# Kernel tuning notes

Hardware: AMD Instinct MI355X
Metric: run time of the kernel (lower is better)

## Reference

```python
import jax, jax.numpy as jnp
import numpy as np

B, G, D, H, L, FFN = 4, 2048, 256, 8, 4, 1024
HD = D // H
BASE = 100.0
MASK_ID = -10.0
LN_EPS = 1e-5


def setup_inputs() -> dict:
    key = jax.random.key(0)
    ks = jax.random.split(key, 18)
    s = 0.02
    f32 = jnp.float32
    return {
        "x": jax.random.uniform(ks[0], (B, G), f32, 0.0, 8.0),
        "gene_emb": jax.random.normal(ks[1], (G, D), f32) * s,
        "Wq": jax.random.normal(ks[2], (L, D, D), f32) * s,
        "bq": jnp.zeros((L, D), f32),
        "Wk": jax.random.normal(ks[3], (L, D, D), f32) * s,
        "bk": jnp.zeros((L, D), f32),
        "Wv": jax.random.normal(ks[4], (L, D, D), f32) * s,
        "bv": jnp.zeros((L, D), f32),
        "ln1_g": jnp.ones((L, D), f32),
        "ln1_b": jnp.zeros((L, D), f32),
        "ln2_g": jnp.ones((L, D), f32),
        "ln2_b": jnp.zeros((L, D), f32),
        "WU": jax.random.normal(ks[5], (L, D, FFN), f32) * s,
        "bU": jnp.zeros((L, FFN), f32),
        "WV": jax.random.normal(ks[6], (L, FFN, D), f32) * s,
        "bV": jnp.zeros((L, D), f32),
        "Wo": jax.random.normal(ks[7], (D, 1), f32) * s,
        "bo": jnp.zeros((1,), f32),
    }


def _ln(x, g, b):
    mu = jnp.mean(x, axis=-1, keepdims=True)
    var = jnp.mean(jnp.square(x - mu), axis=-1, keepdims=True)
    return (x - mu) * jax.lax.rsqrt(var + LN_EPS) * g + b


def _linear_attn(z, Wq, bq, Wk, bk, Wv, bv):
    # feature_type='sqr': phi(u) = u**2; causal (compute_type='iter') linear attention
    q = jnp.square(z @ Wq + bq).reshape(B, G, H, HD)
    k = jnp.square(z @ Wk + bk).reshape(B, G, H, HD)
    v = (z @ Wv + bv).reshape(B, G, H, HD)
    kv = jnp.cumsum(jnp.einsum('bshm,bshd->bshmd', k, v), axis=1)  # prefix sums of k (x) v
    ksum = jnp.cumsum(k, axis=1)
    num = jnp.einsum('bshm,bshmd->bshd', q, kv)
    den = jnp.einsum('bshm,bshm->bsh', q, ksum)
    return (num / (den[..., None] + 1e-16)).reshape(B, G, D)


def reference(x, gene_emb, Wq, bq, Wk, bk, Wv, bv, ln1_g, ln1_b, ln2_g, ln2_b,
              WU, bU, WV, bV, Wo, bo):
    # rotary expression embedding
    inv_freq = 1.0 / BASE ** (jnp.arange(0, D, 2, dtype=jnp.float32) / D)  # [D/2]
    freqs = x[:, :, None] * inv_freq                                       # [B,G,D/2]
    ree = jnp.concatenate([jnp.sin(freqs), jnp.cos(freqs)], axis=-1)       # [B,G,D]
    ree = jnp.where((x == MASK_ID)[..., None], 0.0, ree)
    h = gene_emb[None] + ree
    for l in range(L):
        # pre-LN attention block
        h = h + _linear_attn(_ln(h, ln1_g[l], ln1_b[l]), Wq[l], bq[l], Wk[l], bk[l], Wv[l], bv[l])
        # pre-LN FFN block (exact erf gelu, as torch F.gelu default)
        z = _ln(h, ln2_g[l], ln2_b[l])
        h = h + jax.nn.gelu(z @ WU[l] + bU[l], approximate=False) @ WV[l] + bV[l]
    return (h @ Wo + bo)[..., 0]  # [B,G]
```

## Files before the change

### kernel.cpp

```cpp
#include <hip/hip_runtime.h>
#include <math.h>

constexpr int kB = 4, kG = 2048, kD = 256, kH = 8, kHD = 32, kL = 4, kFFN = 1024;
constexpr int kBG = kB * kG;
constexpr int kCHUNK = 64;
constexpr int kNC = kG / kCHUNK;
constexpr int kSUMSZ = kHD * kHD + kHD;
constexpr int kQKVN = 3 * kD;

typedef __bf16 bf16x8 __attribute__((ext_vector_type(8)));
typedef unsigned short ushort8 __attribute__((ext_vector_type(8)));
typedef float floatx4 __attribute__((ext_vector_type(4)));

__device__ __forceinline__ unsigned short f2bf(float f) {
  unsigned int u = __float_as_uint(f);
  u += 0x7fff + ((u >> 16) & 1);
  return (unsigned short)(u >> 16);
}

__device__ __forceinline__ void load_lds_16(const void* g, void* l) {
  __builtin_amdgcn_global_load_lds((const __attribute__((address_space(1))) void*)g,
                                   (__attribute__((address_space(3))) void*)l,
                                   16, 0, 0);
}

__global__ void embed_kernel(const float* __restrict__ x,
                             const float* __restrict__ ge,
                             float* __restrict__ h) {
  int idx = blockIdx.x * 256 + threadIdx.x;
  int d = idx & (kD - 1);
  int g = (idx >> 8) & (kG - 1);
  int b = idx >> 19;
  float xv = x[b * kG + g];
  int i = d & 127;
  float inv = expf(-(float)i * (4.6051701859880914f / 128.0f));
  float f = xv * inv;
  float r = (d < 128) ? sinf(f) : cosf(f);
  if (xv == -10.0f) r = 0.0f;
  h[idx] = ge[g * kD + d] + r;
}

__global__ void convert_weights_kernel(
    const float* __restrict__ Wq, const float* __restrict__ Wk,
    const float* __restrict__ Wv, const float* __restrict__ WU,
    const float* __restrict__ WV, const float* __restrict__ bq,
    const float* __restrict__ bk, const float* __restrict__ bv,
    unsigned short* __restrict__ Wqkv_t, unsigned short* __restrict__ WU_t,
    unsigned short* __restrict__ WV_t, float* __restrict__ bias_qkv) {
  int blk = blockIdx.x;
  if (blk >= kL * 704) {
    int idx = (blk - kL * 704) * 256 + threadIdx.x;
    if (idx < kL * kQKVN) {
      int l = idx / kQKVN, n = idx % kQKVN;
      float v = (n < 256) ? bq[l * 256 + n]
              : (n < 512) ? bk[l * 256 + n - 256]
                          : bv[l * 256 + n - 512];
      bias_qkv[idx] = v;
    }
    return;
  }
  int l = blk / 704, id = blk % 704;
  const float* src;
  unsigned short* dst;
  int Ksrc, Nsrc, kt, nt;
  if (id < 192) {
    int m = id >> 6, tid = id & 63;
    src = (m == 0 ? Wq : m == 1 ? Wk : Wv) + (size_t)l * 256 * 256;
    dst = Wqkv_t + (size_t)l * kQKVN * 256 + (size_t)m * 256 * 256;
    Ksrc = 256; Nsrc = 256; kt = tid >> 3; nt = tid & 7;
  } else if (id < 448) {
    int tid = id - 192;
    src = WU + (size_t)l * 256 * 1024;
    dst = WU_t + (size_t)l * 1024 * 256;
    Ksrc = 256; Nsrc = 1024; kt = tid >> 5; nt = tid & 31;
  } else {
    int tid = id - 448;
    src = WV + (size_t)l * 1024 * 256;
    dst = WV_t + (size_t)l * 256 * 1024;
    Ksrc = 1024; Nsrc = 256; kt = tid >> 3; nt = tid & 7;
  }
  __shared__ float s[32][33];
  int tx = threadIdx.x & 31, ty = threadIdx.x >> 5;
#pragma unroll
  for (int r = 0; r < 4; r++)
    s[ty + r * 8][tx] = src[(size_t)(kt * 32 + ty + r * 8) * Nsrc + nt * 32 + tx];
  __syncthreads();
#pragma unroll
  for (int r = 0; r < 4; r++)
    dst[(size_t)(nt * 32 + ty + r * 8) * Ksrc + kt * 32 + tx] =
        f2bf(s[tx][ty + r * 8]);
}

__global__ __launch_bounds__(256) void ln_kernel(
    const float* __restrict__ h, const float* __restrict__ gamma,
    const float* __restrict__ beta, unsigned short* __restrict__ z) {
  int w = threadIdx.x >> 6, lane = threadIdx.x & 63;
  size_t row = (size_t)blockIdx.x * 4 + w;
  float4 v = *(const float4*)&h[row * kD + lane * 4];
  float s = v.x + v.y + v.z + v.w;
  float sq = v.x * v.x + v.y * v.y + v.z * v.z + v.w * v.w;
#pragma unroll
  for (int o = 32; o > 0; o >>= 1) {
    s += __shfl_xor(s, o);
    sq += __shfl_xor(sq, o);
  }
  float mu = s * (1.0f / kD);
  float var = sq * (1.0f / kD) - mu * mu;
  float r = rsqrtf(var + 1e-5f);
  float4 g4 = *(const float4*)&gamma[lane * 4];
  float4 b4 = *(const float4*)&beta[lane * 4];
  float y0 = (v.x - mu) * r * g4.x + b4.x;
  float y1 = (v.y - mu) * r * g4.y + b4.y;
  float y2 = (v.z - mu) * r * g4.z + b4.z;
  float y3 = (v.w - mu) * r * g4.w + b4.w;
  unsigned int u0 = (unsigned int)f2bf(y0) | ((unsigned int)f2bf(y1) << 16);
  unsigned int u1 = (unsigned int)f2bf(y2) | ((unsigned int)f2bf(y3) << 16);
  uint2 uu; uu.x = u0; uu.y = u1;
  *(uint2*)&z[row * kD + lane * 4] = uu;
}

template <int EPI>
__global__ __launch_bounds__(256) void mfma_gemm(
    const unsigned short* __restrict__ A, const unsigned short* __restrict__ Bt,
    const float* __restrict__ bias, void* __restrict__ Cout,
    const float* __restrict__ Cres, int M, int N, int K) {
  __shared__ unsigned short As[2][64 * 32];
  __shared__ unsigned short Bs[2][64 * 32];
  const int t = threadIdx.x;
  const int w = t >> 6, lane = t & 63;
  const int bm = blockIdx.y * 64, bn = blockIdx.x * 64;
  const int wm = (w >> 1) * 32, wn = (w & 1) * 32;

  const int srow = lane >> 2;
  const int skof = (lane & 3) * 8;
  const unsigned short* ap = A + (size_t)(bm + w * 16 + srow) * K + skof;
  const unsigned short* bp = Bt + (size_t)(bn + w * 16 + srow) * K + skof;

  floatx4 acc[2][2];
#pragma unroll
  for (int i = 0; i < 2; i++)
#pragma unroll
    for (int j = 0; j < 2; j++) acc[i][j] = (floatx4){0.f, 0.f, 0.f, 0.f};

  const int lm = lane & 15, lq = lane >> 4;
  const int nsteps = K >> 5;

  load_lds_16(ap, &As[0][w * 512]);
  load_lds_16(bp, &Bs[0][w * 512]);
  __syncthreads();

  for (int s = 0; s < nsteps; s++) {
    const int cur = s & 1, nxt = cur ^ 1;
    if (s + 1 < nsteps) {
      load_lds_16(ap + (s + 1) * 32, &As[nxt][w * 512]);
      load_lds_16(bp + (s + 1) * 32, &Bs[nxt][w * 512]);
    }
    const unsigned short* afp = &As[cur][(wm + lm) * 32 + lq * 8];
    const unsigned short* bfp = &Bs[cur][(wn + lm) * 32 + lq * 8];
    bf16x8 af[2], bfr[2];
#pragma unroll
    for (int i = 0; i < 2; i++)
      af[i] = __builtin_bit_cast(bf16x8,
          *reinterpret_cast<const ushort8*>(afp + i * 16 * 32));
#pragma unroll
    for (int j = 0; j < 2; j++)
      bfr[j] = __builtin_bit_cast(bf16x8,
          *reinterpret_cast<const ushort8*>(bfp + j * 16 * 32));
#pragma unroll
    for (int i = 0; i < 2; i++)
#pragma unroll
      for (int j = 0; j < 2; j++)
        acc[i][j] = __builtin_amdgcn_mfma_f32_16x16x32_bf16(af[i], bfr[j],
                                                            acc[i][j], 0, 0, 0);
    __syncthreads();
  }

  const int r0 = bm + wm + lq * 4;
  const int c0 = bn + wn + lm;
#pragma unroll
  for (int j = 0; j < 2; j++) {
    int col = c0 + j * 16;
    float bv = bias[col];
#pragma unroll
    for (int i = 0; i < 2; i++) {
      int rowb = r0 + i * 16;
#pragma unroll
      for (int r = 0; r < 4; r++) {
        int row = rowb + r;
        float v = acc[i][j][r] + bv;
        size_t idx = (size_t)row * N + col;
        if (EPI == 1) {
          ((float*)Cout)[idx] = (col < 512) ? v * v : v;
        } else if (EPI == 2) {
          float g = 0.5f * v * (1.0f + erff(v * 0.70710678118654752f));
          ((unsigned short*)Cout)[idx] = f2bf(g);
        } else {
          ((float*)Cout)[idx] = Cres[idx] + v;
        }
      }
    }
  }
}

__global__ __launch_bounds__(256) void attn_sums_kernel(
    const float* __restrict__ qkv, float* __restrict__ sums) {
  int blk = blockIdx.x;
  int c = blk & (kNC - 1);
  int hh = (blk >> 5) & (kH - 1);
  int b = blk >> 8;
  int g0 = c * kCHUNK;
  __shared__ float ks[kCHUNK][kHD];
  __shared__ float vs[kCHUNK][kHD];
  const float* kbase = qkv + (size_t)(b * kG + g0) * kQKVN + 256 + hh * kHD;
  const float* vbase = qkv + (size_t)(b * kG + g0) * kQKVN + 512 + hh * kHD;
#pragma unroll
  for (int r = 0; r < 2; r++) {
    int e = threadIdx.x + r * 256;
    int i = e >> 3, j = (e & 7) * 4;
    *(float4*)&ks[i][j] = *(const float4*)&kbase[(size_t)i * kQKVN + j];
    *(float4*)&vs[i][j] = *(const float4*)&vbase[(size_t)i * kQKVN + j];
  }
  __syncthreads();
  int m = threadIdx.x >> 3, n0 = (threadIdx.x & 7) * 4;
  float a0 = 0, a1 = 0, a2 = 0, a3 = 0;
  for (int i = 0; i < kCHUNK; i++) {
    float km = ks[i][m];
    float4 v4 = *(const float4*)&vs[i][n0];
    a0 = fmaf(km, v4.x, a0); a1 = fmaf(km, v4.y, a1);
    a2 = fmaf(km, v4.z, a2); a3 = fmaf(km, v4.w, a3);
  }
  float* outp = sums + (size_t)blk * kSUMSZ;
  *(float4*)&outp[m * kHD + n0] = make_float4(a0, a1, a2, a3);
  if (threadIdx.x < kHD) {
    float s = 0;
    for (int i = 0; i < kCHUNK; i++) s += ks[i][threadIdx.x];
    outp[kHD * kHD + threadIdx.x] = s;
  }
}

__global__ void attn_scan_kernel(float* __restrict__ sums) {
  int bh = blockIdx.x / 5, part = blockIdx.x % 5;
  int e = part * 256 + threadIdx.x;
  if (e >= kSUMSZ) return;
  float* base = sums + (size_t)bh * kNC * kSUMSZ + e;
  float v[kNC];
#pragma unroll
  for (int c = 0; c < kNC; c++) v[c] = base[(size_t)c * kSUMSZ];
  float run = 0;
#pragma unroll
  for (int c = 0; c < kNC; c++) {
    float tv = v[c];
    base[(size_t)c * kSUMSZ] = run;
    run += tv;
  }
}

__global__ __launch_bounds__(256) void attn_out_kernel(
    const float* __restrict__ qkv, const float* __restrict__ sums,
    float* __restrict__ h) {
  int blk = blockIdx.x;
  int c = blk & (kNC - 1);
  int hh = (blk >> 5) & (kH - 1);
  int b = blk >> 8;
  int g0 = c * kCHUNK;
  __shared__ float qs[kCHUNK][36];
  __shared__ float ks[kCHUNK][36];
  __shared__ float vs[kCHUNK][36];
  __shared__ float Sf[kHD][kHD];
  __shared__ float ksum[kHD];
  __shared__ float dinv_s[kCHUNK];
  __shared__ float Amat[kCHUNK][68];
  int t = threadIdx.x;
  const float* base = qkv + (size_t)(b * kG + g0) * kQKVN + hh * kHD;
#pragma unroll
  for (int r = 0; r < 2; r++) {
    int e = t + r * 256;
    int i = e >> 3, j = (e & 7) * 4;
    *(float4*)&qs[i][j] = *(const float4*)&base[(size_t)i * kQKVN + j];
    *(float4*)&ks[i][j] = *(const float4*)&base[(size_t)i * kQKVN + 256 + j];
    *(float4*)&vs[i][j] = *(const float4*)&base[(size_t)i * kQKVN + 512 + j];
  }
  const float* sp = sums + (size_t)blk * kSUMSZ;
  *(float4*)&((float*)Sf)[t * 4] = *(const float4*)&sp[t * 4];
  if (t < 8) *(float4*)&ksum[t * 4] = *(const float4*)&sp[kHD * kHD + t * 4];
  __syncthreads();

  {
    int i = t >> 2, jb = t & 3;
    float qr[kHD];
#pragma unroll
    for (int m4 = 0; m4 < kHD / 4; m4++) {
      float4 qv = *(const float4*)&qs[i][m4 * 4];
      qr[m4 * 4 + 0] = qv.x; qr[m4 * 4 + 1] = qv.y;
      qr[m4 * 4 + 2] = qv.z; qr[m4 * 4 + 3] = qv.w;
    }
    float psum = 0.0f;
#pragma unroll
    for (int jj = 0; jj < 16; jj++) {
      int j = jb + jj * 4;
      float s = 0;
#pragma unroll
      for (int m4 = 0; m4 < kHD / 4; m4++) {
        float4 kv = *(const float4*)&ks[j][m4 * 4];
        s = fmaf(qr[m4 * 4 + 0], kv.x, s);
        s = fmaf(qr[m4 * 4 + 1], kv.y, s);
        s = fmaf(qr[m4 * 4 + 2], kv.z, s);
        s = fmaf(qr[m4 * 4 + 3], kv.w, s);
      }
      Amat[i][j] = s;
      if (j <= i) psum += s;
    }
    psum += __shfl_xor(psum, 1);
    psum += __shfl_xor(psum, 2);
    if (jb == 0) {
      float dk = 0;
#pragma unroll
      for (int m = 0; m < kHD; m++) dk = fmaf(qr[m], ksum[m], dk);
      dinv_s[i] = 1.0f / (psum + dk + 1e-16f);
    }
  }
  __syncthreads();

  float* hbase = h + (size_t)(b * kG + g0) * kD + hh * kHD;
#pragma unroll
  for (int uu = 0; uu < 2; uu++) {
    int u = t + uu * 256;
    int i = u >> 3, n0 = (u & 7) * 4;
    float ax = 0, ay = 0, az = 0, aw = 0;
#pragma unroll
    for (int m = 0; m < kHD; m++) {
      float qm = qs[i][m];
      float4 s4 = *(const float4*)&Sf[m][n0];
      ax = fmaf(qm, s4.x, ax); ay = fmaf(qm, s4.y, ay);
      az = fmaf(qm, s4.z, az); aw = fmaf(qm, s4.w, aw);
    }
    for (int j = 0; j <= i; j++) {
      float w = Amat[i][j];
      float4 vv = *(const float4*)&vs[j][n0];
      ax = fmaf(w, vv.x, ax); ay = fmaf(w, vv.y, ay);
      az = fmaf(w, vv.z, az); aw = fmaf(w, vv.w, aw);
    }
    float dinv = dinv_s[i];
    float* hp = hbase + (size_t)i * kD + n0;
    float4 old = *(const float4*)hp;
    *(float4*)hp = make_float4(old.x + ax * dinv, old.y + ay * dinv,
                               old.z + az * dinv, old.w + aw * dinv);
  }
}

__global__ __launch_bounds__(256) void final_kernel(
    const float* __restrict__ h, const float* __restrict__ Wo,
    const float* __restrict__ bo, float* __restrict__ out) {
  int w = threadIdx.x >> 6, lane = threadIdx.x & 63;
  size_t row = (size_t)blockIdx.x * 4 + w;
  float4 hv = *(const float4*)&h[row * kD + lane * 4];
  float4 wv = *(const float4*)&Wo[lane * 4];
  float s = hv.x * wv.x + hv.y * wv.y + hv.z * wv.z + hv.w * wv.w;
#pragma unroll
  for (int o = 32; o > 0; o >>= 1) s += __shfl_xor(s, o);
  if (lane == 0) out[row] = s + bo[0];
}

extern "C" void kernel_launch(void* const* d_in, const int* in_sizes, int n_in,
                              void* d_out, int out_size, void* d_ws, size_t ws_size,
                              hipStream_t stream) {
  const float* x    = (const float*)d_in[0];
  const float* ge   = (const float*)d_in[1];
  const float* Wq   = (const float*)d_in[2];
  const float* bq   = (const float*)d_in[3];
  const float* Wk   = (const float*)d_in[4];
  const float* bk   = (const float*)d_in[5];
  const float* Wv   = (const float*)d_in[6];
  const float* bv   = (const float*)d_in[7];
  const float* ln1g = (const float*)d_in[8];
  const float* ln1b = (const float*)d_in[9];
  const float* ln2g = (const float*)d_in[10];
  const float* ln2b = (const float*)d_in[11];
  const float* WU   = (const float*)d_in[12];
  const float* bU   = (const float*)d_in[13];
  const float* WV   = (const float*)d_in[14];
  const float* bV   = (const float*)d_in[15];
  const float* Wo   = (const float*)d_in[16];
  const float* bo   = (const float*)d_in[17];
  float* out = (float*)d_out;

  float* ws = (float*)d_ws;
  float*          h       = ws;
  unsigned short* zb      = (unsigned short*)(ws + 2097152);
  float*          qkv     = ws + 3145728;
  unsigned short* u       = (unsigned short*)qkv;
  float*          sums    = ws + 9437184;
  unsigned short* Wqkv_t  = (unsigned short*)(ws + 10518528);
  unsigned short* WU_t    = (unsigned short*)(ws + 10911744);
  unsigned short* WV_t    = (unsigned short*)(ws + 11436032);
  float*          bias_qkv= ws + 11960320;

  dim3 blk256(256);
  convert_weights_kernel<<<kL * 704 + 12, blk256, 0, stream>>>(
      Wq, Wk, Wv, WU, WV, bq, bk, bv, Wqkv_t, WU_t, WV_t, bias_qkv);
  embed_kernel<<<kBG * kD / 256, blk256, 0, stream>>>(x, ge, h);
  for (int l = 0; l < kL; l++) {
    ln_kernel<<<kBG / 4, blk256, 0, stream>>>(h, ln1g + l * kD, ln1b + l * kD, zb);
    mfma_gemm<1><<<dim3(kQKVN / 64, kBG / 64), blk256, 0, stream>>>(
        zb, Wqkv_t + (size_t)l * kQKVN * kD, bias_qkv + l * kQKVN, qkv, nullptr,
        kBG, kQKVN, kD);
    attn_sums_kernel<<<kB * kH * kNC, blk256, 0, stream>>>(qkv, sums);
    attn_scan_kernel<<<kB * kH * 5, blk256, 0, stream>>>(sums);
    attn_out_kernel<<<kB * kH * kNC, blk256, 0, stream>>>(qkv, sums, h);
    ln_kernel<<<kBG / 4, blk256, 0, stream>>>(h, ln2g + l * kD, ln2b + l * kD, zb);
    mfma_gemm<2><<<dim3(kFFN / 64, kBG / 64), blk256, 0, stream>>>(
        zb, WU_t + (size_t)l * kFFN * kD, bU + l * kFFN, u, nullptr,
        kBG, kFFN, kD);
    mfma_gemm<3><<<dim3(kD / 64, kBG / 64), blk256, 0, stream>>>(
        u, WV_t + (size_t)l * kD * kFFN, bV + l * kD, h, h,
        kBG, kD, kFFN);
  }
  final_kernel<<<kBG / 4, blk256, 0, stream>>>(h, Wo, bo, out);
}
```

Baseline: 425.2 us.

## Fuse LayerNorm into QKV and FFN-up GEMMs with full-width row tiles

Replaces the separate LayerNorm kernels and the tiled 64x64 GEMMs with a fused kernel. Each block normalizes 32 rows of h into LDS as bf16, then multiplies them against the full output width (768 or 1024 columns), reading B fragments straight from global memory. This drops the bf16 z round trip and two launches per layer. In exchange the grid shrinks to 256 blocks, and weights are re-read from global or L2 by every block without LDS staging.

After: 481.4 us. 1.13x slower.

```diff
diff --git a/kernel.cpp b/kernel.cpp
--- a/kernel.cpp
+++ b/kernel.cpp
@@ -91,32 +91,99 @@
         f2bf(s[tx][ty + r * 8]);
 }
 
-__global__ __launch_bounds__(256) void ln_kernel(
-    const float* __restrict__ h, const float* __restrict__ gamma,
-    const float* __restrict__ beta, unsigned short* __restrict__ z) {
-  int w = threadIdx.x >> 6, lane = threadIdx.x & 63;
-  size_t row = (size_t)blockIdx.x * 4 + w;
-  float4 v = *(const float4*)&h[row * kD + lane * 4];
-  float s = v.x + v.y + v.z + v.w;
-  float sq = v.x * v.x + v.y * v.y + v.z * v.z + v.w * v.w;
-#pragma unroll
-  for (int o = 32; o > 0; o >>= 1) {
-    s += __shfl_xor(s, o);
-    sq += __shfl_xor(sq, o);
-  }
-  float mu = s * (1.0f / kD);
-  float var = sq * (1.0f / kD) - mu * mu;
-  float r = rsqrtf(var + 1e-5f);
-  float4 g4 = *(const float4*)&gamma[lane * 4];
-  float4 b4 = *(const float4*)&beta[lane * 4];
-  float y0 = (v.x - mu) * r * g4.x + b4.x;
-  float y1 = (v.y - mu) * r * g4.y + b4.y;
-  float y2 = (v.z - mu) * r * g4.z + b4.z;
-  float y3 = (v.w - mu) * r * g4.w + b4.w;
-  unsigned int u0 = (unsigned int)f2bf(y0) | ((unsigned int)f2bf(y1) << 16);
-  unsigned int u1 = (unsigned int)f2bf(y2) | ((unsigned int)f2bf(y3) << 16);
-  uint2 uu; uu.x = u0; uu.y = u1;
-  *(uint2*)&z[row * kD + lane * 4] = uu;
+template <int EPI, int NW, int JT>
+__global__ __launch_bounds__(NW * 64) void ln_mfma_gemm(
+    const float* __restrict__ hsrc, const unsigned short* __restrict__ Bt,
+    const float* __restrict__ bias, const float* __restrict__ gamma,
+    const float* __restrict__ beta, void* __restrict__ Cout) {
+  constexpr int N = NW * JT * 16;
+  constexpr int AST = 264;
+  constexpr int TPR = NW * 2;
+  constexpr int CPT = 256 / TPR;
+  __shared__ unsigned short As[32 * AST];
+  const int t = threadIdx.x;
+  const int w = t >> 6, lane = t & 63;
+  const int r0 = blockIdx.x * 32;
+
+  {
+    int row = t / TPR, p = t % TPR;
+    const float* hp = hsrc + (size_t)(r0 + row) * 256 + p * CPT;
+    float va[CPT];
+#pragma unroll
+    for (int i = 0; i < CPT / 4; i++)
+      *(float4*)&va[i * 4] = *(const float4*)&hp[i * 4];
+    float s = 0.f, sq = 0.f;
+#pragma unroll
+    for (int i = 0; i < CPT; i++) { s += va[i]; sq += va[i] * va[i]; }
+#pragma unroll
+    for (int o = 1; o < TPR; o <<= 1) {
+      s += __shfl_xor(s, o);
+      sq += __shfl_xor(sq, o);
+    }
+    float mu = s * (1.0f / kD);
+    float var = sq * (1.0f / kD) - mu * mu;
+    float rr = rsqrtf(var + 1e-5f);
+    unsigned short* dst = &As[row * AST + p * CPT];
+#pragma unroll
+    for (int gi = 0; gi < CPT / 8; gi++) {
+      ushort8 pk;
+#pragma unroll
+      for (int e = 0; e < 8; e++) {
+        int cc = gi * 8 + e;
+        float y = (va[cc] - mu) * rr * gamma[p * CPT + cc] + beta[p * CPT + cc];
+        pk[e] = f2bf(y);
+      }
+      *(ushort8*)&dst[gi * 8] = pk;
+    }
+  }
+  __syncthreads();
+
+  const int lm = lane & 15, lq = lane >> 4;
+  const int cbase = w * (JT * 16);
+  floatx4 acc[2][JT];
+#pragma unroll
+  for (int i = 0; i < 2; i++)
+#pragma unroll
+    for (int j = 0; j < JT; j++) acc[i][j] = (floatx4){0.f, 0.f, 0.f, 0.f};
+
+  const unsigned short* bptr = Bt + (size_t)(cbase + lm) * 256 + lq * 8;
+  const unsigned short* afp = &As[lm * AST + lq * 8];
+#pragma unroll
+  for (int ks = 0; ks < 8; ks++) {
+    const int k0 = ks * 32;
+    bf16x8 af0 = __builtin_bit_cast(bf16x8,
+        *reinterpret_cast<const ushort8*>(afp + k0));
+    bf16x8 af1 = __builtin_bit_cast(bf16x8,
+        *reinterpret_cast<const ushort8*>(afp + 16 * AST + k0));
+#pragma unroll
+    for (int j = 0; j < JT; j++) {
+      bf16x8 bf = __builtin_bit_cast(bf16x8,
+          *reinterpret_cast<const ushort8*>(bptr + (size_t)(j * 16) * 256 + k0));
+      acc[0][j] = __builtin_amdgcn_mfma_f32_16x16x32_bf16(af0, bf, acc[0][j], 0, 0, 0);
+      acc[1][j] = __builtin_amdgcn_mfma_f32_16x16x32_bf16(af1, bf, acc[1][j], 0, 0, 0);
+    }
+  }
+
+#pragma unroll
+  for (int j = 0; j < JT; j++) {
+    int col = cbase + j * 16 + lm;
+    float bv = bias[col];
+#pragma unroll
+    for (int i = 0; i < 2; i++) {
+#pragma unroll
+      for (int r = 0; r < 4; r++) {
+        int row = r0 + i * 16 + lq * 4 + r;
+        float v = acc[i][j][r] + bv;
+        if (EPI == 1) {
+          if (col < 512) v = v * v;
+          ((float*)Cout)[(size_t)row * N + col] = v;
+        } else {
+          float g = 0.5f * v * (1.0f + erff(v * 0.70710678118654752f));
+          ((unsigned short*)Cout)[(size_t)row * N + col] = f2bf(g);
+        }
+      }
+    }
+  }
 }
 
 template <int EPI>
@@ -189,14 +256,7 @@
         int row = rowb + r;
         float v = acc[i][j][r] + bv;
         size_t idx = (size_t)row * N + col;
-        if (EPI == 1) {
-          ((float*)Cout)[idx] = (col < 512) ? v * v : v;
-        } else if (EPI == 2) {
-          float g = 0.5f * v * (1.0f + erff(v * 0.70710678118654752f));
-          ((unsigned short*)Cout)[idx] = f2bf(g);
-        } else {
-          ((float*)Cout)[idx] = Cres[idx] + v;
-        }
+        ((float*)Cout)[idx] = Cres[idx] + v;
       }
     }
   }
@@ -386,7 +446,6 @@
 
   float* ws = (float*)d_ws;
   float*          h       = ws;
-  unsigned short* zb      = (unsigned short*)(ws + 2097152);
   float*          qkv     = ws + 3145728;
   unsigned short* u       = (unsigned short*)qkv;
   float*          sums    = ws + 9437184;
@@ -400,17 +459,15 @@
       Wq, Wk, Wv, WU, WV, bq, bk, bv, Wqkv_t, WU_t, WV_t, bias_qkv);
   embed_kernel<<<kBG * kD / 256, blk256, 0, stream>>>(x, ge, h);
   for (int l = 0; l < kL; l++) {
-    ln_kernel<<<kBG / 4, blk256, 0, stream>>>(h, ln1g + l * kD, ln1b + l * kD, zb);
-    mfma_gemm<1><<<dim3(kQKVN / 64, kBG / 64), blk256, 0, stream>>>(
-        zb, Wqkv_t + (size_t)l * kQKVN * kD, bias_qkv + l * kQKVN, qkv, nullptr,
-        kBG, kQKVN, kD);
+    ln_mfma_gemm<1, 4, 12><<<kBG / 32, dim3(256), 0, stream>>>(
+        h, Wqkv_t + (size_t)l * kQKVN * kD, bias_qkv + l * kQKVN,
+        ln1g + l * kD, ln1b + l * kD, qkv);
     attn_sums_kernel<<<kB * kH * kNC, blk256, 0, stream>>>(qkv, sums);
     attn_scan_kernel<<<kB * kH * 5, blk256, 0, stream>>>(sums);
     attn_out_kernel<<<kB * kH * kNC, blk256, 0, stream>>>(qkv, sums, h);
-    ln_kernel<<<kBG / 4, blk256, 0, stream>>>(h, ln2g + l * kD, ln2b + l * kD, zb);
-    mfma_gemm<2><<<dim3(kFFN / 64, kBG / 64), blk256, 0, stream>>>(
-        zb, WU_t + (size_t)l * kFFN * kD, bU + l * kFFN, u, nullptr,
-        kBG, kFFN, kD);
+    ln_mfma_gemm<2, 8, 8><<<kBG / 32, dim3(512), 0, stream>>>(
+        h, WU_t + (size_t)l * kFFN * kD, bU + l * kFFN,
+        ln2g + l * kD, ln2b + l * kD, u);
     mfma_gemm<3><<<dim3(kD / 64, kBG / 64), blk256, 0, stream>>>(
         u, WV_t + (size_t)l * kD * kFFN, bV + l * kD, h, h,
         kBG, kD, kFFN);
```

## Store squared q/k as bf16 and compute intra-chunk attention scores with MFMA

Applied to the files above, without the earlier changes.

The QKV GEMM epilogue now writes the squared q and k as bf16 into a separate buffer and v as fp32 into another, which roughly halves the bytes written for q/k and read later by the attention kernels. attn_out_kernel computes the 64x64 intra-chunk q·k score matrix with bf16 MFMA instructions instead of scalar FMAs, and derives the denominator row sums with lane shuffles. The trade-off is precision: squared q/k rounded to bf16 feed the numerator and denominator of the linear attention.

New measurement: 405.1 us. 4.7% less time.

```diff
diff --git a/kernel.cpp b/kernel.cpp
--- a/kernel.cpp
+++ b/kernel.cpp
@@ -16,6 +16,9 @@
   unsigned int u = __float_as_uint(f);
   u += 0x7fff + ((u >> 16) & 1);
   return (unsigned short)(u >> 16);
+}
+__device__ __forceinline__ float bf2f(unsigned short u) {
+  return __uint_as_float(((unsigned int)u) << 16);
 }
 
 __device__ __forceinline__ void load_lds_16(const void* g, void* l) {
@@ -123,7 +126,8 @@
 __global__ __launch_bounds__(256) void mfma_gemm(
     const unsigned short* __restrict__ A, const unsigned short* __restrict__ Bt,
     const float* __restrict__ bias, void* __restrict__ Cout,
-    const float* __restrict__ Cres, int M, int N, int K) {
+    void* __restrict__ Cout2, const float* __restrict__ Cres,
+    int M, int N, int K) {
   __shared__ unsigned short As[2][64 * 32];
   __shared__ unsigned short Bs[2][64 * 32];
   const int t = threadIdx.x;
@@ -188,13 +192,17 @@
       for (int r = 0; r < 4; r++) {
         int row = rowb + r;
         float v = acc[i][j][r] + bv;
-        size_t idx = (size_t)row * N + col;
         if (EPI == 1) {
-          ((float*)Cout)[idx] = (col < 512) ? v * v : v;
+          if (col < 512) {
+            ((unsigned short*)Cout)[(size_t)row * 512 + col] = f2bf(v * v);
+          } else {
+            ((float*)Cout2)[(size_t)row * 256 + col - 512] = v;
+          }
         } else if (EPI == 2) {
           float g = 0.5f * v * (1.0f + erff(v * 0.70710678118654752f));
-          ((unsigned short*)Cout)[idx] = f2bf(g);
+          ((unsigned short*)Cout)[(size_t)row * N + col] = f2bf(g);
         } else {
+          size_t idx = (size_t)row * N + col;
           ((float*)Cout)[idx] = Cres[idx] + v;
         }
       }
@@ -203,7 +211,8 @@
 }
 
 __global__ __launch_bounds__(256) void attn_sums_kernel(
-    const float* __restrict__ qkv, float* __restrict__ sums) {
+    const unsigned short* __restrict__ qkb, const float* __restrict__ vbuf,
+    float* __restrict__ sums) {
   int blk = blockIdx.x;
   int c = blk & (kNC - 1);
   int hh = (blk >> 5) & (kH - 1);
@@ -211,17 +220,23 @@
   int g0 = c * kCHUNK;
   __shared__ float ks[kCHUNK][kHD];
   __shared__ float vs[kCHUNK][kHD];
-  const float* kbase = qkv + (size_t)(b * kG + g0) * kQKVN + 256 + hh * kHD;
-  const float* vbase = qkv + (size_t)(b * kG + g0) * kQKVN + 512 + hh * kHD;
+  int t = threadIdx.x;
+  {
+    int i = t >> 2, j8 = (t & 3) * 8;
+    ushort8 kv = *(const ushort8*)&qkb[(size_t)(b * kG + g0 + i) * 512 + 256 +
+                                       hh * kHD + j8];
+#pragma unroll
+    for (int e = 0; e < 8; e++) ks[i][j8 + e] = bf2f(kv[e]);
+  }
 #pragma unroll
   for (int r = 0; r < 2; r++) {
-    int e = threadIdx.x + r * 256;
+    int e = t + r * 256;
     int i = e >> 3, j = (e & 7) * 4;
-    *(float4*)&ks[i][j] = *(const float4*)&kbase[(size_t)i * kQKVN + j];
-    *(float4*)&vs[i][j] = *(const float4*)&vbase[(size_t)i * kQKVN + j];
+    *(float4*)&vs[i][j] =
+        *(const float4*)&vbuf[(size_t)(b * kG + g0 + i) * kD + hh * kHD + j];
   }
   __syncthreads();
-  int m = threadIdx.x >> 3, n0 = (threadIdx.x & 7) * 4;
+  int m = t >> 3, n0 = (t & 7) * 4;
   float a0 = 0, a1 = 0, a2 = 0, a3 = 0;
   for (int i = 0; i < kCHUNK; i++) {
     float km = ks[i][m];
@@ -231,10 +246,10 @@
   }
   float* outp = sums + (size_t)blk * kSUMSZ;
   *(float4*)&outp[m * kHD + n0] = make_float4(a0, a1, a2, a3);
-  if (threadIdx.x < kHD) {
+  if (t < kHD) {
     float s = 0;
-    for (int i = 0; i < kCHUNK; i++) s += ks[i][threadIdx.x];
-    outp[kHD * kHD + threadIdx.x] = s;
+    for (int i = 0; i < kCHUNK; i++) s += ks[i][t];
+    outp[kHD * kHD + t] = s;
   }
 }
 
@@ -256,29 +271,33 @@
 }
 
 __global__ __launch_bounds__(256) void attn_out_kernel(
-    const float* __restrict__ qkv, const float* __restrict__ sums,
-    float* __restrict__ h) {
+    const unsigned short* __restrict__ qkb, const float* __restrict__ vbuf,
+    const float* __restrict__ sums, float* __restrict__ h) {
   int blk = blockIdx.x;
   int c = blk & (kNC - 1);
   int hh = (blk >> 5) & (kH - 1);
   int b = blk >> 8;
   int g0 = c * kCHUNK;
-  __shared__ float qs[kCHUNK][36];
-  __shared__ float ks[kCHUNK][36];
+  __shared__ unsigned short qb[kCHUNK * 40];
+  __shared__ unsigned short kb[kCHUNK * 40];
   __shared__ float vs[kCHUNK][36];
   __shared__ float Sf[kHD][kHD];
   __shared__ float ksum[kHD];
   __shared__ float dinv_s[kCHUNK];
   __shared__ float Amat[kCHUNK][68];
   int t = threadIdx.x;
-  const float* base = qkv + (size_t)(b * kG + g0) * kQKVN + hh * kHD;
+  {
+    int i = t >> 2, j8 = (t & 3) * 8;
+    const unsigned short* qrow = qkb + (size_t)(b * kG + g0 + i) * 512 + hh * kHD;
+    *(ushort8*)&qb[i * 40 + j8] = *(const ushort8*)&qrow[j8];
+    *(ushort8*)&kb[i * 40 + j8] = *(const ushort8*)&qrow[256 + j8];
+  }
 #pragma unroll
   for (int r = 0; r < 2; r++) {
     int e = t + r * 256;
     int i = e >> 3, j = (e & 7) * 4;
-    *(float4*)&qs[i][j] = *(const float4*)&base[(size_t)i * kQKVN + j];
-    *(float4*)&ks[i][j] = *(const float4*)&base[(size_t)i * kQKVN + 256 + j];
-    *(float4*)&vs[i][j] = *(const float4*)&base[(size_t)i * kQKVN + 512 + j];
+    *(float4*)&vs[i][j] =
+        *(const float4*)&vbuf[(size_t)(b * kG + g0 + i) * kD + hh * kHD + j];
   }
   const float* sp = sums + (size_t)blk * kSUMSZ;
   *(float4*)&((float*)Sf)[t * 4] = *(const float4*)&sp[t * 4];
@@ -286,37 +305,39 @@
   __syncthreads();
 
   {
-    int i = t >> 2, jb = t & 3;
-    float qr[kHD];
-#pragma unroll
-    for (int m4 = 0; m4 < kHD / 4; m4++) {
-      float4 qv = *(const float4*)&qs[i][m4 * 4];
-      qr[m4 * 4 + 0] = qv.x; qr[m4 * 4 + 1] = qv.y;
-      qr[m4 * 4 + 2] = qv.z; qr[m4 * 4 + 3] = qv.w;
-    }
-    float psum = 0.0f;
-#pragma unroll
-    for (int jj = 0; jj < 16; jj++) {
-      int j = jb + jj * 4;
-      float s = 0;
-#pragma unroll
-      for (int m4 = 0; m4 < kHD / 4; m4++) {
-        float4 kv = *(const float4*)&ks[j][m4 * 4];
-        s = fmaf(qr[m4 * 4 + 0], kv.x, s);
-        s = fmaf(qr[m4 * 4 + 1], kv.y, s);
-        s = fmaf(qr[m4 * 4 + 2], kv.z, s);
-        s = fmaf(qr[m4 * 4 + 3], kv.w, s);
+    const int w = t >> 6, lane = t & 63;
+    const int lm = lane & 15, lq = lane >> 4;
+    bf16x8 afr = __builtin_bit_cast(bf16x8,
+        *reinterpret_cast<const ushort8*>(&qb[(16 * w + lm) * 40 + lq * 8]));
+    floatx4 pacc[4];
+#pragma unroll
+    for (int jt = 0; jt < 4; jt++) {
+      bf16x8 bfr = __builtin_bit_cast(bf16x8,
+          *reinterpret_cast<const ushort8*>(&kb[(16 * jt + lm) * 40 + lq * 8]));
+      pacc[jt] = __builtin_amdgcn_mfma_f32_16x16x32_bf16(
+          afr, bfr, (floatx4){0.f, 0.f, 0.f, 0.f}, 0, 0, 0);
+    }
+#pragma unroll
+    for (int jt = 0; jt < 4; jt++)
+#pragma unroll
+      for (int r = 0; r < 4; r++)
+        Amat[16 * w + lq * 4 + r][16 * jt + lm] = pacc[jt][r];
+#pragma unroll
+    for (int r = 0; r < 4; r++) {
+      int row = 16 * w + lq * 4 + r;
+      float ps = 0.f;
+#pragma unroll
+      for (int jt = 0; jt < 4; jt++) {
+        int j = 16 * jt + lm;
+        ps += (j <= row) ? pacc[jt][r] : 0.f;
       }
-      Amat[i][j] = s;
-      if (j <= i) psum += s;
-    }
-    psum += __shfl_xor(psum, 1);
-    psum += __shfl_xor(psum, 2);
-    if (jb == 0) {
-      float dk = 0;
-#pragma unroll
-      for (int m = 0; m < kHD; m++) dk = fmaf(qr[m], ksum[m], dk);
-      dinv_s[i] = 1.0f / (psum + dk + 1e-16f);
+      ps += bf2f(qb[row * 40 + lm]) * ksum[lm];
+      ps += bf2f(qb[row * 40 + lm + 16]) * ksum[lm + 16];
+      ps += __shfl_xor(ps, 1);
+      ps += __shfl_xor(ps, 2);
+      ps += __shfl_xor(ps, 4);
+      ps += __shfl_xor(ps, 8);
+      if (lm == 0) dinv_s[row] = 1.0f / (ps + 1e-16f);
     }
   }
   __syncthreads();
@@ -329,7 +350,7 @@
     float ax = 0, ay = 0, az = 0, aw = 0;
 #pragma unroll
     for (int m = 0; m < kHD; m++) {
-      float qm = qs[i][m];
+      float qm = bf2f(qb[i * 40 + m]);
       float4 s4 = *(const float4*)&Sf[m][n0];
       ax = fmaf(qm, s4.x, ax); ay = fmaf(qm, s4.y, ay);
       az = fmaf(qm, s4.z, az); aw = fmaf(qm, s4.w, aw);
@@ -387,8 +408,9 @@
   float* ws = (float*)d_ws;
   float*          h       = ws;
   unsigned short* zb      = (unsigned short*)(ws + 2097152);
-  float*          qkv     = ws + 3145728;
-  unsigned short* u       = (unsigned short*)qkv;
+  unsigned short* qkb     = (unsigned short*)(ws + 3145728);
+  float*          vbuf    = ws + 5242880;
+  unsigned short* u       = (unsigned short*)(ws + 3145728);
   float*          sums    = ws + 9437184;
   unsigned short* Wqkv_t  = (unsigned short*)(ws + 10518528);
   unsigned short* WU_t    = (unsigned short*)(ws + 10911744);
@@ -402,17 +424,17 @@
   for (int l = 0; l < kL; l++) {
     ln_kernel<<<kBG / 4, blk256, 0, stream>>>(h, ln1g + l * kD, ln1b + l * kD, zb);
     mfma_gemm<1><<<dim3(kQKVN / 64, kBG / 64), blk256, 0, stream>>>(
-        zb, Wqkv_t + (size_t)l * kQKVN * kD, bias_qkv + l * kQKVN, qkv, nullptr,
-        kBG, kQKVN, kD);
-    attn_sums_kernel<<<kB * kH * kNC, blk256, 0, stream>>>(qkv, sums);
+        zb, Wqkv_t + (size_t)l * kQKVN * kD, bias_qkv + l * kQKVN, qkb, vbuf,
+        nullptr, kBG, kQKVN, kD);
+    attn_sums_kernel<<<kB * kH * kNC, blk256, 0, stream>>>(qkb, vbuf, sums);
     attn_scan_kernel<<<kB * kH * 5, blk256, 0, stream>>>(sums);
-    attn_out_kernel<<<kB * kH * kNC, blk256, 0, stream>>>(qkv, sums, h);
+    attn_out_kernel<<<kB * kH * kNC, blk256, 0, stream>>>(qkb, vbuf, sums, h);
     ln_kernel<<<kBG / 4, blk256, 0, stream>>>(h, ln2g + l * kD, ln2b + l * kD, zb);
     mfma_gemm<2><<<dim3(kFFN / 64, kBG / 64), blk256, 0, stream>>>(
-        zb, WU_t + (size_t)l * kFFN * kD, bU + l * kFFN, u, nullptr,
+        zb, WU_t + (size_t)l * kFFN * kD, bU + l * kFFN, u, nullptr, nullptr,
         kBG, kFFN, kD);
     mfma_gemm<3><<<dim3(kD / 64, kBG / 64), blk256, 0, stream>>>(
-        u, WV_t + (size_t)l * kD * kFFN, bV + l * kD, h, h,
+        u, WV_t + (size_t)l * kD * kFFN, bV + l * kD, h, nullptr, h,
         kBG, kD, kFFN);
   }
   final_kernel<<<kBG / 4, blk256, 0, stream>>>(h, Wo, bo, out);
```
